# Kernel optimization log

Measured on AMD Instinct MI355X. Metric: run time of the kernel, lower is better.

The kernel has to match this reference:

```python
import jax, jax.numpy as jnp
import numpy as np

DIM = 256
GROUPS = 32
EPS = 1e-6


def setup_inputs() -> dict:
    key = jax.random.key(0)
    ks = jax.random.split(key, 7)
    B, C, H, W = 4, DIM, 64, 64
    s = 1.0 / np.sqrt(C)
    return {
        "x": jax.random.normal(ks[0], (B, C, H, W), dtype=jnp.float32),
        "gamma": jnp.ones((C,), dtype=jnp.float32),
        "beta": jnp.zeros((C,), dtype=jnp.float32),
        "w_qkv": jax.random.normal(ks[1], (3 * C, C), dtype=jnp.float32) * s,
        "b_qkv": jnp.zeros((3 * C,), dtype=jnp.float32),
        "w_proj": jax.random.normal(ks[2], (C, C), dtype=jnp.float32) * s,
        "b_proj": jnp.zeros((C,), dtype=jnp.float32),
    }


def reference(x, gamma, beta, w_qkv, b_qkv, w_proj, b_proj):
    B, C, H, W = x.shape
    N = H * W
    scale = jnp.asarray(C, x.dtype) ** 0.5

    # GroupNorm(32, C, eps=1e-6, affine)
    h = x.reshape(B, GROUPS, C // GROUPS, N)
    mu = h.mean(axis=(2, 3), keepdims=True)
    var = h.var(axis=(2, 3), keepdims=True)
    h = (h - mu) * jax.lax.rsqrt(var + EPS)
    h = h.reshape(B, C, N) * gamma[None, :, None] + beta[None, :, None]

    # 1x1 conv QKV == channel matmul
    qkv = jnp.einsum('oc,bcn->bon', w_qkv, h) + b_qkv[None, :, None]  # (B,3C,N)
    qkv = qkv.reshape(B, 3, C, N)
    q = qkv[:, 0].transpose(0, 2, 1)  # (B,N,C)
    k = qkv[:, 1].transpose(0, 2, 1)
    v = qkv[:, 2].transpose(0, 2, 1)

    attn = jnp.einsum('bqc,bkc->bqk', q, k) / scale  # (B,N,N)
    attn = jax.nn.softmax(attn, axis=-1)
    out = jnp.einsum('bqk,bkc->bqc', attn, v)  # (B,N,C)

    out = out.transpose(0, 2, 1)  # (B,C,N)
    out = jnp.einsum('oc,bcn->bon', w_proj, out) + b_proj[None, :, None]
    return x + out.reshape(B, C, H, W)
```

## Files before the change

### kernel.cpp

```cpp
#include <hip/hip_runtime.h>
#include <stdint.h>

#define DIM 256
#define NPOS 4096
#define NB 4
#define GROUPS 32

typedef __attribute__((ext_vector_type(8))) short short8;
typedef __attribute__((ext_vector_type(4))) short short4v;
typedef __attribute__((ext_vector_type(4))) float f32x4;
typedef __attribute__((ext_vector_type(16))) float f32x16;
typedef __attribute__((ext_vector_type(2))) unsigned int u32x2;
typedef __attribute__((ext_vector_type(4))) unsigned int u32x4;

__device__ __forceinline__ short f2b(float f) {
  unsigned u = __float_as_uint(f);
  unsigned r = (u + 0x7fffu + ((u >> 16) & 1u)) >> 16;
  return (short)r;
}

__device__ __forceinline__ void gl16(const short* g, char* lds) {
  __builtin_amdgcn_global_load_lds((const __attribute__((address_space(1))) void*)g,
                                   (__attribute__((address_space(3))) void*)lds, 16, 0, 0);
}

__global__ void k_convert_w(const float* __restrict__ wq, const float* __restrict__ wp,
                            short* __restrict__ wqb, short* __restrict__ wpb) {
  int i = blockIdx.x * 256 + threadIdx.x;
  if (i < 768 * 256) wqb[i] = f2b(wq[i]);
  if (i < 256 * 256) wpb[i] = f2b(wp[i]);
}

__global__ void k_gn_stats(const float* __restrict__ x, float* __restrict__ stats) {
  int bg = blockIdx.x;
  const float4* b4 = (const float4*)(x + (size_t)bg * 8 * NPOS);
  float s = 0.f, ss = 0.f;
  for (int i = threadIdx.x; i < 8192; i += 256) {
    float4 v = b4[i];
    s  += v.x + v.y + v.z + v.w;
    ss += v.x * v.x + v.y * v.y + v.z * v.z + v.w * v.w;
  }
  #pragma unroll
  for (int m = 1; m < 64; m <<= 1) { s += __shfl_xor(s, m, 64); ss += __shfl_xor(ss, m, 64); }
  __shared__ float red[8];
  int wid = threadIdx.x >> 6;
  if ((threadIdx.x & 63) == 0) { red[wid * 2] = s; red[wid * 2 + 1] = ss; }
  __syncthreads();
  if (threadIdx.x == 0) {
    float S = red[0] + red[2] + red[4] + red[6];
    float SS = red[1] + red[3] + red[5] + red[7];
    float mean = S / 32768.f;
    float var = SS / 32768.f - mean * mean;
    stats[bg * 2] = mean;
    stats[bg * 2 + 1] = rsqrtf(var + 1e-6f);
  }
}

__global__ void k_gn_apply(const float* __restrict__ x, const float* __restrict__ stats,
                           const float* __restrict__ gamma, const float* __restrict__ beta,
                           short* __restrict__ ht) {
  int ct = blockIdx.x, nt = blockIdx.y, b = blockIdx.z;
  int c0 = ct * 64, n0 = nt * 64;
  __shared__ short lt[64 * 72];
  int t = threadIdx.x;
  #pragma unroll
  for (int p = 0; p < 4; ++p) {
    int row = (t >> 4) + p * 16;
    int colb = (t & 15) * 4;
    int c = c0 + row;
    float mean = stats[(b * GROUPS + (c >> 3)) * 2];
    float rstd = stats[(b * GROUPS + (c >> 3)) * 2 + 1];
    float ga = gamma[c], be = beta[c];
    float4 v = *(const float4*)(x + ((size_t)(b * DIM + c)) * NPOS + n0 + colb);
    short4v o;
    o.x = f2b((v.x - mean) * rstd * ga + be);
    o.y = f2b((v.y - mean) * rstd * ga + be);
    o.z = f2b((v.z - mean) * rstd * ga + be);
    o.w = f2b((v.w - mean) * rstd * ga + be);
    *(short4v*)&lt[row * 72 + colb] = o;
  }
  __syncthreads();
  #pragma unroll
  for (int p = 0; p < 2; ++p) {
    int nr = (t >> 3) + p * 32;
    int ch = t & 7;
    short8 o;
    #pragma unroll
    for (int j = 0; j < 8; ++j) o[j] = lt[(ch * 8 + j) * 72 + nr];
    *(short8*)(ht + ((size_t)(b * NPOS + n0 + nr)) * DIM + c0 + ch * 8) = o;
  }
}

template <int MODE>
__launch_bounds__(256, 2)
__global__ void k_gemm(const short* __restrict__ A, const short* __restrict__ Bm,
                       const float* __restrict__ bias,
                       short* __restrict__ qb, short* __restrict__ kb, short* __restrict__ vtb,
                       const float* __restrict__ resid, float* __restrict__ outf) {
  const int K = 256;
  int b = blockIdx.z;
  int m0 = blockIdx.x * 128, n0 = blockIdx.y * 128;
  const short* Ap = (MODE == 0) ? A + (size_t)b * NPOS * K : A;
  const short* Bp = (MODE == 0) ? Bm : Bm + (size_t)b * NPOS * K;

  __shared__ short As[128 * 64], Bs[128 * 64];
  int t = threadIdx.x;
  int lane = t & 63, wid = t >> 6;
  int wm = wid >> 1, wn = wid & 1;
  f32x4 acc[4][4] = {};

  for (int kt = 0; kt < 4; ++kt) {
    int k0 = kt * 64;
    short8 av[4], bv[4];
    #pragma unroll
    for (int p = 0; p < 4; ++p) {
      int ci = t + p * 256;
      int row = ci >> 3, ch = ci & 7;
      av[p] = *(const short8*)(Ap + (size_t)(m0 + row) * K + k0 + ch * 8);
      bv[p] = *(const short8*)(Bp + (size_t)(n0 + row) * K + k0 + ch * 8);
    }
    __syncthreads();
    #pragma unroll
    for (int p = 0; p < 4; ++p) {
      int ci = t + p * 256;
      int row = ci >> 3, ch = ci & 7;
      int off = (row * 128 + ch * 16) ^ ((row & 7) << 4);
      *(short8*)((char*)As + off) = av[p];
      *(short8*)((char*)Bs + off) = bv[p];
    }
    __syncthreads();
    #pragma unroll
    for (int ks = 0; ks < 2; ++ks) {
      short8 af[4], bf[4];
      int inner = ks * 64 + (lane >> 4) * 16;
      #pragma unroll
      for (int mi = 0; mi < 4; ++mi) {
        int row = wm * 64 + mi * 16 + (lane & 15);
        af[mi] = *(short8*)((char*)As + ((row * 128 + inner) ^ ((row & 7) << 4)));
      }
      #pragma unroll
      for (int ni = 0; ni < 4; ++ni) {
        int row = wn * 64 + ni * 16 + (lane & 15);
        bf[ni] = *(short8*)((char*)Bs + ((row * 128 + inner) ^ ((row & 7) << 4)));
      }
      #pragma unroll
      for (int mi = 0; mi < 4; ++mi)
        #pragma unroll
        for (int ni = 0; ni < 4; ++ni)
          acc[mi][ni] = __builtin_amdgcn_mfma_f32_16x16x32_bf16(af[mi], bf[ni], acc[mi][ni], 0, 0, 0);
    }
  }

  #pragma unroll
  for (int mi = 0; mi < 4; ++mi)
    #pragma unroll
    for (int ni = 0; ni < 4; ++ni) {
      int gcol = n0 + wn * 64 + ni * 16 + (lane & 15);
      #pragma unroll
      for (int r = 0; r < 4; ++r) {
        int grow = m0 + wm * 64 + mi * 16 + (lane >> 4) * 4 + r;
        if (MODE == 0) {
          float v = acc[mi][ni][r] + bias[gcol];
          short h = f2b(v);
          if (gcol < 256)       qb[((size_t)b * NPOS + grow) * DIM + gcol] = h;
          else if (gcol < 512)  kb[((size_t)b * NPOS + grow) * DIM + gcol - 256] = h;
          else                  vtb[((size_t)b * DIM + gcol - 512) * NPOS + grow] = h;
        } else {
          float v = acc[mi][ni][r] + bias[grow];
          size_t idx = ((size_t)b * DIM + grow) * NPOS + gcol;
          outf[idx] = v + resid[idx];
        }
      }
    }
}

__launch_bounds__(256, 1)
__global__ void k_flash(const short* __restrict__ qb, const short* __restrict__ kb,
                        const short* __restrict__ vtb, short* __restrict__ ob) {
  __shared__ __align__(16) char smem[131072];

  int i = blockIdx.x;
  int xcd = i & 7, slot = i >> 3;
  int b = xcd >> 1;
  int bx = slot * 2 + (xcd & 1);
  int q0 = bx * 64;

  int t = threadIdx.x, lane = t & 63, wid = t >> 6;
  int q = lane & 31, hi = lane >> 5;
  int qs = wid & 1, h = wid >> 1;

  const short* kbB = kb + (size_t)b * NPOS * DIM;
  const short* vbB = vtb + (size_t)b * DIM * NPOS;

  short8 qf[16];
  {
    int qrow = q0 + qs * 32 + q;
    const short* qp = qb + ((size_t)b * NPOS + qrow) * DIM + hi * 8;
    #pragma unroll
    for (int s = 0; s < 16; ++s) {
      short8 v = *(const short8*)(qp + s * 16);
      #pragma unroll
      for (int j = 0; j < 8; ++j) {
        float f = __uint_as_float(((unsigned)(unsigned short)v[j]) << 16) * 0.0625f;
        v[j] = f2b(f);
      }
      qf[s] = v;
    }
  }

  unsigned su = h * 16384u + qs * 8192u;
  const short* srcK[8];
  const short* srcV[8];
  {
    int l5 = lane >> 5, l31 = lane & 31;
    #pragma unroll
    for (int j = 0; j < 8; ++j) {
      int r = qs * 16 + j * 2 + l5;
      int colb = (l31 * 16) ^ ((r & 7) << 4);
      srcK[j] = kbB + (size_t)(h * 2048 + r) * DIM + (colb >> 1);
      int vr = qs * 128 + j * 16 + (lane >> 2);
      int vcol = ((lane & 3) * 16) ^ ((vr & 6) << 3);
      srcV[j] = vbB + (size_t)vr * NPOS + h * 2048 + (vcol >> 1);
    }
  }

  f32x16 oacc[8] = {};
  float m = -1e30f, l = 0.f;

  const int NIT = 64;
  int buf = 0;
  #pragma unroll
  for (int j = 0; j < 8; ++j) {
    gl16(srcK[j], smem + su + j * 1024u);
    gl16(srcV[j], smem + 65536u + su + j * 1024u);
  }
  __syncthreads();

  const unsigned kx = (unsigned)((q & 7) << 4);
  const unsigned vx = (unsigned)((q & 6) << 3);

  for (int it = 0; it < NIT; ++it) {
    if (it + 1 < NIT) {
      size_t ko = (size_t)(it + 1) * 32 * DIM;
      int vo = (it + 1) * 32;
      unsigned nb = (unsigned)(buf ^ 1) * 32768u + su;
      #pragma unroll
      for (int j = 0; j < 8; ++j) {
        gl16(srcK[j] + ko, smem + nb + j * 1024u);
        gl16(srcV[j] + vo, smem + 65536u + nb + j * 1024u);
      }
    }

    const char* kl = smem + (unsigned)buf * 32768u + h * 16384u;
    const char* vl = smem + 65536u + (unsigned)buf * 32768u + h * 16384u;
    f32x16 sacc = {};
    #pragma unroll
    for (int s = 0; s < 16; ++s) {
      short8 kf = *(const short8*)(kl + q * 512u + ((s * 32u + hi * 16u) ^ kx));
      sacc = __builtin_amdgcn_mfma_f32_32x32x16_bf16(kf, qf[s], sacc, 0, 0, 0);
    }

    float mx = sacc[0];
    #pragma unroll
    for (int r = 1; r < 16; ++r) mx = fmaxf(mx, sacc[r]);
    mx = fmaxf(mx, __shfl_xor(mx, 32, 64));
    if (!__all(mx <= m + 8.f)) {
      float mn = fmaxf(m, mx);
      float al = __expf(m - mn);
      m = mn; l *= al;
      #pragma unroll
      for (int dt = 0; dt < 8; ++dt)
        #pragma unroll
        for (int r = 0; r < 16; ++r) oacc[dt][r] *= al;
    }
    float p_[16];
    float ts = 0.f;
    #pragma unroll
    for (int r = 0; r < 16; ++r) { p_[r] = __expf(sacc[r] - m); ts += p_[r]; }
    ts += __shfl_xor(ts, 32, 64);
    l += ts;

    unsigned w0, w1, w2, w3, w4, w5, w6, w7;
    asm("v_cvt_pk_bf16_f32 %0, %1, %2" : "=v"(w0) : "v"(p_[0]),  "v"(p_[1]));
    asm("v_cvt_pk_bf16_f32 %0, %1, %2" : "=v"(w1) : "v"(p_[2]),  "v"(p_[3]));
    asm("v_cvt_pk_bf16_f32 %0, %1, %2" : "=v"(w2) : "v"(p_[4]),  "v"(p_[5]));
    asm("v_cvt_pk_bf16_f32 %0, %1, %2" : "=v"(w3) : "v"(p_[6]),  "v"(p_[7]));
    asm("v_cvt_pk_bf16_f32 %0, %1, %2" : "=v"(w4) : "v"(p_[8]),  "v"(p_[9]));
    asm("v_cvt_pk_bf16_f32 %0, %1, %2" : "=v"(w5) : "v"(p_[10]), "v"(p_[11]));
    asm("v_cvt_pk_bf16_f32 %0, %1, %2" : "=v"(w6) : "v"(p_[12]), "v"(p_[13]));
    asm("v_cvt_pk_bf16_f32 %0, %1, %2" : "=v"(w7) : "v"(p_[14]), "v"(p_[15]));
    asm("v_permlane32_swap_b32 %0, %1" : "+v"(w0), "+v"(w2));
    asm("v_permlane32_swap_b32 %0, %1" : "+v"(w1), "+v"(w3));
    asm("v_permlane32_swap_b32 %0, %1" : "+v"(w4), "+v"(w6));
    asm("v_permlane32_swap_b32 %0, %1" : "+v"(w5), "+v"(w7));
    short8 pf0 = __builtin_bit_cast(short8, (u32x4){w0, w1, w2, w3});
    short8 pf1 = __builtin_bit_cast(short8, (u32x4){w4, w5, w6, w7});

    #pragma unroll
    for (int dt = 0; dt < 8; ++dt) {
      unsigned vrow = (dt * 32u + q) * 64u;
      short8 vf0 = *(const short8*)(vl + vrow + ((hi * 16u) ^ vx));
      short8 vf1 = *(const short8*)(vl + vrow + ((32u + hi * 16u) ^ vx));
      oacc[dt] = __builtin_amdgcn_mfma_f32_32x32x16_bf16(vf0, pf0, oacc[dt], 0, 0, 0);
      oacc[dt] = __builtin_amdgcn_mfma_f32_32x32x16_bf16(vf1, pf1, oacc[dt], 0, 0, 0);
    }
    __syncthreads();
    buf ^= 1;
  }

  float* lmm = (float*)(smem + 100352);
  float* lml = lmm + 128;
  if (lane < 32) { lmm[(qs * 2 + h) * 32 + q] = m; lml[(qs * 2 + h) * 32 + q] = l; }
  __syncthreads();
  float mo = lmm[(qs * 2 + (h ^ 1)) * 32 + q];
  float lo = lml[(qs * 2 + (h ^ 1)) * 32 + q];
  float M = fmaxf(m, mo);
  float al = __expf(m - M);
  float Lf = l * al + lo * __expf(mo - M);
  float iL = 1.f / Lf;

  float* sc32 = (float*)smem;
  short* sc16 = (short*)(smem + 66560);
  if (h == 0) {
    #pragma unroll
    for (int dt = 0; dt < 8; ++dt)
      #pragma unroll
      for (int r = 0; r < 16; ++r) {
        int d = dt * 32 + (r & 3) + 8 * (r >> 2) + 4 * hi;
        sc32[qs * 8224 + q * 257 + d] = oacc[dt][r] * al;
      }
  }
  __syncthreads();
  if (h == 1) {
    #pragma unroll
    for (int dt = 0; dt < 8; ++dt)
      #pragma unroll
      for (int r = 0; r < 16; ++r) {
        int d = dt * 32 + (r & 3) + 8 * (r >> 2) + 4 * hi;
        float v = (sc32[qs * 8224 + q * 257 + d] + oacc[dt][r] * al) * iL;
        sc16[qs * 8256 + q * 258 + d] = f2b(v);
      }
  }
  __syncthreads();
  {
    int row = t >> 2;
    const short* src = sc16 + (row >> 5) * 8256 + (row & 31) * 258 + (t & 3) * 64;
    short* dst = ob + ((size_t)b * NPOS + q0 + row) * DIM + (t & 3) * 64;
    #pragma unroll
    for (int j = 0; j < 8; ++j)
      *(short8*)(dst + j * 8) = *(const short8*)(src + j * 8);
  }
}

extern "C" void kernel_launch(void* const* d_in, const int* in_sizes, int n_in,
                              void* d_out, int out_size, void* d_ws, size_t ws_size,
                              hipStream_t stream) {
  const float* x     = (const float*)d_in[0];
  const float* gamma = (const float*)d_in[1];
  const float* beta  = (const float*)d_in[2];
  const float* wqkv  = (const float*)d_in[3];
  const float* bqkv  = (const float*)d_in[4];
  const float* wproj = (const float*)d_in[5];
  const float* bproj = (const float*)d_in[6];
  float* out = (float*)d_out;

  char* ws = (char*)d_ws;
  float* stats = (float*)ws;
  short* wqb = (short*)(ws + 1024);
  short* wpb = (short*)(ws + 1024 + 393216);
  size_t off = 1024 + 393216 + 131072;
  const size_t SZ = (size_t)NB * NPOS * DIM * sizeof(short);
  short* ht   = (short*)(ws + off); off += SZ;
  short* qbuf = (short*)(ws + off); off += SZ;
  short* kbuf = (short*)(ws + off); off += SZ;
  short* vtb  = (short*)(ws + off); off += SZ;
  short* obuf = ht;

  k_convert_w<<<768, 256, 0, stream>>>(wqkv, wproj, wqb, wpb);
  k_gn_stats<<<128, 256, 0, stream>>>(x, stats);
  k_gn_apply<<<dim3(4, 64, NB), 256, 0, stream>>>(x, stats, gamma, beta, ht);
  k_gemm<0><<<dim3(32, 6, NB), 256, 0, stream>>>(ht, wqb, bqkv, qbuf, kbuf, vtb, nullptr, nullptr);
  k_flash<<<dim3(256), 256, 0, stream>>>(qbuf, kbuf, vtb, obuf);
  k_gemm<1><<<dim3(2, 32, NB), 256, 0, stream>>>(wpb, obuf, bproj, nullptr, nullptr, nullptr, x, out);
}
```

Baseline: 176.1 us.

## Split flash attention head dimension across two wave groups with 512-thread blocks

Doubles the flash-attention block to 8 waves, splitting the V/output head dimension into two halves so each wave holds 4 output accumulator tiles instead of 8. K/V tile loads are redistributed across all 512 threads, and the final merge and store are adapted to the new layout. This lowers per-wave register pressure and raises waves per CU for better latency hiding. In exchange, each QK^T score tile and its softmax are computed twice, once by each half. The launch_bounds minimum-blocks hint of 2 cannot be met given the 128KB shared-memory allocation.

```diff
diff --git a/kernel.cpp b/kernel.cpp
--- a/kernel.cpp
+++ b/kernel.cpp
@@ -174,7 +174,7 @@
     }
 }
 
-__launch_bounds__(256, 1)
+__launch_bounds__(512, 2)
 __global__ void k_flash(const short* __restrict__ qb, const short* __restrict__ kb,
                         const short* __restrict__ vtb, short* __restrict__ ob) {
   __shared__ __align__(16) char smem[131072];
@@ -187,7 +187,7 @@
 
   int t = threadIdx.x, lane = t & 63, wid = t >> 6;
   int q = lane & 31, hi = lane >> 5;
-  int qs = wid & 1, h = wid >> 1;
+  int qs = wid & 1, h = (wid >> 1) & 1, ds = wid >> 2;
 
   const short* kbB = kb + (size_t)b * NPOS * DIM;
   const short* vbB = vtb + (size_t)b * DIM * NPOS;
@@ -208,31 +208,32 @@
     }
   }
 
-  unsigned su = h * 16384u + qs * 8192u;
-  const short* srcK[8];
-  const short* srcV[8];
-  {
-    int l5 = lane >> 5, l31 = lane & 31;
-    #pragma unroll
-    for (int j = 0; j < 8; ++j) {
-      int r = qs * 16 + j * 2 + l5;
-      int colb = (l31 * 16) ^ ((r & 7) << 4);
-      srcK[j] = kbB + (size_t)(h * 2048 + r) * DIM + (colb >> 1);
-      int vr = qs * 128 + j * 16 + (lane >> 2);
-      int vcol = ((lane & 3) * 16) ^ ((vr & 6) << 3);
-      srcV[j] = vbB + (size_t)vr * NPOS + h * 2048 + (vcol >> 1);
-    }
-  }
-
-  f32x16 oacc[8] = {};
+  const short* srcK[4];
+  const short* srcV[4];
+  unsigned dstK[4], dstV[4];
+  #pragma unroll
+  for (int j = 0; j < 4; ++j) {
+    int c = wid * 4 + j;
+    int ch = c >> 4;
+    int kr = (c & 15) * 2 + (lane >> 5);
+    int kcol = ((lane & 31) * 16) ^ ((kr & 7) << 4);
+    srcK[j] = kbB + (size_t)(ch * 2048 + kr) * DIM + (kcol >> 1);
+    int dr = (c & 15) * 16 + (lane >> 2);
+    int vcol = ((lane & 3) * 16) ^ ((dr & 6) << 3);
+    srcV[j] = vbB + (size_t)dr * NPOS + ch * 2048 + (vcol >> 1);
+    dstK[j] = (unsigned)c * 1024u;
+    dstV[j] = 65536u + (unsigned)c * 1024u;
+  }
+
+  f32x16 oacc[4] = {};
   float m = -1e30f, l = 0.f;
 
   const int NIT = 64;
   int buf = 0;
   #pragma unroll
-  for (int j = 0; j < 8; ++j) {
-    gl16(srcK[j], smem + su + j * 1024u);
-    gl16(srcV[j], smem + 65536u + su + j * 1024u);
+  for (int j = 0; j < 4; ++j) {
+    gl16(srcK[j], smem + dstK[j]);
+    gl16(srcV[j], smem + dstV[j]);
   }
   __syncthreads();
 
@@ -243,11 +244,11 @@
     if (it + 1 < NIT) {
       size_t ko = (size_t)(it + 1) * 32 * DIM;
       int vo = (it + 1) * 32;
-      unsigned nb = (unsigned)(buf ^ 1) * 32768u + su;
-      #pragma unroll
-      for (int j = 0; j < 8; ++j) {
-        gl16(srcK[j] + ko, smem + nb + j * 1024u);
-        gl16(srcV[j] + vo, smem + 65536u + nb + j * 1024u);
+      unsigned nb = (unsigned)(buf ^ 1) * 32768u;
+      #pragma unroll
+      for (int j = 0; j < 4; ++j) {
+        gl16(srcK[j] + ko, smem + nb + dstK[j]);
+        gl16(srcV[j] + vo, smem + nb + dstV[j]);
       }
     }
 
@@ -269,7 +270,7 @@
       float al = __expf(m - mn);
       m = mn; l *= al;
       #pragma unroll
-      for (int dt = 0; dt < 8; ++dt)
+      for (int dt = 0; dt < 4; ++dt)
         #pragma unroll
         for (int r = 0; r < 16; ++r) oacc[dt][r] *= al;
     }
@@ -297,12 +298,12 @@
     short8 pf1 = __builtin_bit_cast(short8, (u32x4){w4, w5, w6, w7});
 
     #pragma unroll
-    for (int dt = 0; dt < 8; ++dt) {
-      unsigned vrow = (dt * 32u + q) * 64u;
+    for (int dtl = 0; dtl < 4; ++dtl) {
+      unsigned vrow = ((ds * 4 + dtl) * 32u + q) * 64u;
       short8 vf0 = *(const short8*)(vl + vrow + ((hi * 16u) ^ vx));
       short8 vf1 = *(const short8*)(vl + vrow + ((32u + hi * 16u) ^ vx));
-      oacc[dt] = __builtin_amdgcn_mfma_f32_32x32x16_bf16(vf0, pf0, oacc[dt], 0, 0, 0);
-      oacc[dt] = __builtin_amdgcn_mfma_f32_32x32x16_bf16(vf1, pf1, oacc[dt], 0, 0, 0);
+      oacc[dtl] = __builtin_amdgcn_mfma_f32_32x32x16_bf16(vf0, pf0, oacc[dtl], 0, 0, 0);
+      oacc[dtl] = __builtin_amdgcn_mfma_f32_32x32x16_bf16(vf1, pf1, oacc[dtl], 0, 0, 0);
     }
     __syncthreads();
     buf ^= 1;
@@ -310,7 +311,7 @@
 
   float* lmm = (float*)(smem + 100352);
   float* lml = lmm + 128;
-  if (lane < 32) { lmm[(qs * 2 + h) * 32 + q] = m; lml[(qs * 2 + h) * 32 + q] = l; }
+  if (ds == 0 && lane < 32) { lmm[(qs * 2 + h) * 32 + q] = m; lml[(qs * 2 + h) * 32 + q] = l; }
   __syncthreads();
   float mo = lmm[(qs * 2 + (h ^ 1)) * 32 + q];
   float lo = lml[(qs * 2 + (h ^ 1)) * 32 + q];
@@ -323,31 +324,31 @@
   short* sc16 = (short*)(smem + 66560);
   if (h == 0) {
     #pragma unroll
-    for (int dt = 0; dt < 8; ++dt)
+    for (int dtl = 0; dtl < 4; ++dtl)
       #pragma unroll
       for (int r = 0; r < 16; ++r) {
-        int d = dt * 32 + (r & 3) + 8 * (r >> 2) + 4 * hi;
-        sc32[qs * 8224 + q * 257 + d] = oacc[dt][r] * al;
+        int d = (ds * 4 + dtl) * 32 + (r & 3) + 8 * (r >> 2) + 4 * hi;
+        sc32[qs * 8224 + q * 257 + d] = oacc[dtl][r] * al;
       }
   }
   __syncthreads();
   if (h == 1) {
     #pragma unroll
-    for (int dt = 0; dt < 8; ++dt)
+    for (int dtl = 0; dtl < 4; ++dtl)
       #pragma unroll
       for (int r = 0; r < 16; ++r) {
-        int d = dt * 32 + (r & 3) + 8 * (r >> 2) + 4 * hi;
-        float v = (sc32[qs * 8224 + q * 257 + d] + oacc[dt][r] * al) * iL;
+        int d = (ds * 4 + dtl) * 32 + (r & 3) + 8 * (r >> 2) + 4 * hi;
+        float v = (sc32[qs * 8224 + q * 257 + d] + oacc[dtl][r] * al) * iL;
         sc16[qs * 8256 + q * 258 + d] = f2b(v);
       }
   }
   __syncthreads();
   {
-    int row = t >> 2;
-    const short* src = sc16 + (row >> 5) * 8256 + (row & 31) * 258 + (t & 3) * 64;
-    short* dst = ob + ((size_t)b * NPOS + q0 + row) * DIM + (t & 3) * 64;
-    #pragma unroll
-    for (int j = 0; j < 8; ++j)
+    int row = t >> 3;
+    const short* src = sc16 + (row >> 5) * 8256 + (row & 31) * 258 + (t & 7) * 32;
+    short* dst = ob + ((size_t)b * NPOS + q0 + row) * DIM + (t & 7) * 32;
+    #pragma unroll
+    for (int j = 0; j < 4; ++j)
       *(short8*)(dst + j * 8) = *(const short8*)(src + j * 8);
   }
 }
@@ -380,6 +381,6 @@
   k_gn_stats<<<128, 256, 0, stream>>>(x, stats);
   k_gn_apply<<<dim3(4, 64, NB), 256, 0, stream>>>(x, stats, gamma, beta, ht);
   k_gemm<0><<<dim3(32, 6, NB), 256, 0, stream>>>(ht, wqb, bqkv, qbuf, kbuf, vtb, nullptr, nullptr);
-  k_flash<<<dim3(256), 256, 0, stream>>>(qbuf, kbuf, vtb, obuf);
+  k_flash<<<dim3(256), 512, 0, stream>>>(qbuf, kbuf, vtb, obuf);
   k_gemm<1><<<dim3(2, 32, NB), 256, 0, stream>>>(wpb, obuf, bproj, nullptr, nullptr, nullptr, x, out);
 }
```

After: 182.5 us. 3.6% more time.

## Load V fragments directly into registers instead of staging through LDS

Applied to the files above, without the earlier changes.

The V tile is no longer staged in shared memory via global_load_lds. Each lane now loads its own V MFMA operands straight from global memory into a double-buffered register array (vA/vB), and the loop is unrolled by two to alternate the buffers. The aim is to remove the LDS traffic for V reads and shrink shared memory use. In exchange, register pressure grows by 32 short8 values, and the per-lane global V loads are less coalesced (16-byte chunks strided by NPOS rows).

```diff
diff --git a/kernel.cpp b/kernel.cpp
--- a/kernel.cpp
+++ b/kernel.cpp
@@ -177,7 +177,7 @@
 __launch_bounds__(256, 1)
 __global__ void k_flash(const short* __restrict__ qb, const short* __restrict__ kb,
                         const short* __restrict__ vtb, short* __restrict__ ob) {
-  __shared__ __align__(16) char smem[131072];
+  __shared__ __align__(16) char smem[101376];
 
   int i = blockIdx.x;
   int xcd = i & 7, slot = i >> 3;
@@ -210,7 +210,6 @@
 
   unsigned su = h * 16384u + qs * 8192u;
   const short* srcK[8];
-  const short* srcV[8];
   {
     int l5 = lane >> 5, l31 = lane & 31;
     #pragma unroll
@@ -218,95 +217,97 @@
       int r = qs * 16 + j * 2 + l5;
       int colb = (l31 * 16) ^ ((r & 7) << 4);
       srcK[j] = kbB + (size_t)(h * 2048 + r) * DIM + (colb >> 1);
-      int vr = qs * 128 + j * 16 + (lane >> 2);
-      int vcol = ((lane & 3) * 16) ^ ((vr & 6) << 3);
-      srcV[j] = vbB + (size_t)vr * NPOS + h * 2048 + (vcol >> 1);
-    }
-  }
+    }
+  }
+
+  const short* vbase = vbB + (size_t)q * NPOS + h * 2048 + hi * 8;
 
   f32x16 oacc[8] = {};
   float m = -1e30f, l = 0.f;
+  short8 vA[16], vB[16];
 
   const int NIT = 64;
   int buf = 0;
   #pragma unroll
-  for (int j = 0; j < 8; ++j) {
-    gl16(srcK[j], smem + su + j * 1024u);
-    gl16(srcV[j], smem + 65536u + su + j * 1024u);
+  for (int j = 0; j < 8; ++j) gl16(srcK[j], smem + su + j * 1024u);
+  #pragma unroll
+  for (int dt = 0; dt < 8; ++dt) {
+    vA[2 * dt]     = *(const short8*)(vbase + (size_t)dt * 32 * NPOS);
+    vA[2 * dt + 1] = *(const short8*)(vbase + (size_t)dt * 32 * NPOS + 16);
   }
   __syncthreads();
 
   const unsigned kx = (unsigned)((q & 7) << 4);
-  const unsigned vx = (unsigned)((q & 6) << 3);
-
-  for (int it = 0; it < NIT; ++it) {
-    if (it + 1 < NIT) {
-      size_t ko = (size_t)(it + 1) * 32 * DIM;
-      int vo = (it + 1) * 32;
-      unsigned nb = (unsigned)(buf ^ 1) * 32768u + su;
-      #pragma unroll
-      for (int j = 0; j < 8; ++j) {
-        gl16(srcK[j] + ko, smem + nb + j * 1024u);
-        gl16(srcV[j] + vo, smem + 65536u + nb + j * 1024u);
-      }
-    }
-
-    const char* kl = smem + (unsigned)buf * 32768u + h * 16384u;
-    const char* vl = smem + 65536u + (unsigned)buf * 32768u + h * 16384u;
-    f32x16 sacc = {};
-    #pragma unroll
-    for (int s = 0; s < 16; ++s) {
-      short8 kf = *(const short8*)(kl + q * 512u + ((s * 32u + hi * 16u) ^ kx));
-      sacc = __builtin_amdgcn_mfma_f32_32x32x16_bf16(kf, qf[s], sacc, 0, 0, 0);
-    }
-
-    float mx = sacc[0];
-    #pragma unroll
-    for (int r = 1; r < 16; ++r) mx = fmaxf(mx, sacc[r]);
-    mx = fmaxf(mx, __shfl_xor(mx, 32, 64));
-    if (!__all(mx <= m + 8.f)) {
-      float mn = fmaxf(m, mx);
-      float al = __expf(m - mn);
-      m = mn; l *= al;
-      #pragma unroll
-      for (int dt = 0; dt < 8; ++dt)
-        #pragma unroll
-        for (int r = 0; r < 16; ++r) oacc[dt][r] *= al;
-    }
-    float p_[16];
-    float ts = 0.f;
-    #pragma unroll
-    for (int r = 0; r < 16; ++r) { p_[r] = __expf(sacc[r] - m); ts += p_[r]; }
-    ts += __shfl_xor(ts, 32, 64);
-    l += ts;
-
-    unsigned w0, w1, w2, w3, w4, w5, w6, w7;
-    asm("v_cvt_pk_bf16_f32 %0, %1, %2" : "=v"(w0) : "v"(p_[0]),  "v"(p_[1]));
-    asm("v_cvt_pk_bf16_f32 %0, %1, %2" : "=v"(w1) : "v"(p_[2]),  "v"(p_[3]));
-    asm("v_cvt_pk_bf16_f32 %0, %1, %2" : "=v"(w2) : "v"(p_[4]),  "v"(p_[5]));
-    asm("v_cvt_pk_bf16_f32 %0, %1, %2" : "=v"(w3) : "v"(p_[6]),  "v"(p_[7]));
-    asm("v_cvt_pk_bf16_f32 %0, %1, %2" : "=v"(w4) : "v"(p_[8]),  "v"(p_[9]));
-    asm("v_cvt_pk_bf16_f32 %0, %1, %2" : "=v"(w5) : "v"(p_[10]), "v"(p_[11]));
-    asm("v_cvt_pk_bf16_f32 %0, %1, %2" : "=v"(w6) : "v"(p_[12]), "v"(p_[13]));
-    asm("v_cvt_pk_bf16_f32 %0, %1, %2" : "=v"(w7) : "v"(p_[14]), "v"(p_[15]));
-    asm("v_permlane32_swap_b32 %0, %1" : "+v"(w0), "+v"(w2));
-    asm("v_permlane32_swap_b32 %0, %1" : "+v"(w1), "+v"(w3));
-    asm("v_permlane32_swap_b32 %0, %1" : "+v"(w4), "+v"(w6));
-    asm("v_permlane32_swap_b32 %0, %1" : "+v"(w5), "+v"(w7));
-    short8 pf0 = __builtin_bit_cast(short8, (u32x4){w0, w1, w2, w3});
-    short8 pf1 = __builtin_bit_cast(short8, (u32x4){w4, w5, w6, w7});
-
-    #pragma unroll
-    for (int dt = 0; dt < 8; ++dt) {
-      unsigned vrow = (dt * 32u + q) * 64u;
-      short8 vf0 = *(const short8*)(vl + vrow + ((hi * 16u) ^ vx));
-      short8 vf1 = *(const short8*)(vl + vrow + ((32u + hi * 16u) ^ vx));
-      oacc[dt] = __builtin_amdgcn_mfma_f32_32x32x16_bf16(vf0, pf0, oacc[dt], 0, 0, 0);
-      oacc[dt] = __builtin_amdgcn_mfma_f32_32x32x16_bf16(vf1, pf1, oacc[dt], 0, 0, 0);
-    }
-    __syncthreads();
-    buf ^= 1;
-  }
+
+#define FITER(IT, VC, VN)                                                          \
+  {                                                                                \
+    if ((IT) + 1 < NIT) {                                                          \
+      size_t ko = (size_t)((IT) + 1) * 32 * DIM;                                   \
+      unsigned nb = (unsigned)(buf ^ 1) * 32768u + su;                             \
+      _Pragma("unroll")                                                            \
+      for (int j = 0; j < 8; ++j) gl16(srcK[j] + ko, smem + nb + j * 1024u);       \
+      const short* vb2 = vbase + ((IT) + 1) * 32;                                  \
+      _Pragma("unroll")                                                            \
+      for (int dt = 0; dt < 8; ++dt) {                                             \
+        VN[2 * dt]     = *(const short8*)(vb2 + (size_t)dt * 32 * NPOS);           \
+        VN[2 * dt + 1] = *(const short8*)(vb2 + (size_t)dt * 32 * NPOS + 16);      \
+      }                                                                            \
+    }                                                                              \
+    const char* kl = smem + (unsigned)buf * 32768u + h * 16384u;                   \
+    f32x16 sacc = {};                                                              \
+    _Pragma("unroll")                                                              \
+    for (int s = 0; s < 16; ++s) {                                                 \
+      short8 kf = *(const short8*)(kl + q * 512u + ((s * 32u + hi * 16u) ^ kx));   \
+      sacc = __builtin_amdgcn_mfma_f32_32x32x16_bf16(kf, qf[s], sacc, 0, 0, 0);    \
+    }                                                                              \
+    float mx = sacc[0];                                                            \
+    _Pragma("unroll")                                                              \
+    for (int r = 1; r < 16; ++r) mx = fmaxf(mx, sacc[r]);                          \
+    mx = fmaxf(mx, __shfl_xor(mx, 32, 64));                                        \
+    if (!__all(mx <= m + 8.f)) {                                                   \
+      float mn = fmaxf(m, mx);                                                     \
+      float al = __expf(m - mn);                                                   \
+      m = mn; l *= al;                                                             \
+      _Pragma("unroll")                                                            \
+      for (int dt = 0; dt < 8; ++dt)                                               \
+        _Pragma("unroll")                                                          \
+        for (int r = 0; r < 16; ++r) oacc[dt][r] *= al;                            \
+    }                                                                              \
+    float p_[16];                                                                  \
+    float ts = 0.f;                                                                \
+    _Pragma("unroll")                                                              \
+    for (int r = 0; r < 16; ++r) { p_[r] = __expf(sacc[r] - m); ts += p_[r]; }     \
+    ts += __shfl_xor(ts, 32, 64);                                                  \
+    l += ts;                                                                       \
+    unsigned w0, w1, w2, w3, w4, w5, w6, w7;                                       \
+    asm("v_cvt_pk_bf16_f32 %0, %1, %2" : "=v"(w0) : "v"(p_[0]),  "v"(p_[1]));      \
+    asm("v_cvt_pk_bf16_f32 %0, %1, %2" : "=v"(w1) : "v"(p_[2]),  "v"(p_[3]));      \
+    asm("v_cvt_pk_bf16_f32 %0, %1, %2" : "=v"(w2) : "v"(p_[4]),  "v"(p_[5]));      \
+    asm("v_cvt_pk_bf16_f32 %0, %1, %2" : "=v"(w3) : "v"(p_[6]),  "v"(p_[7]));      \
+    asm("v_cvt_pk_bf16_f32 %0, %1, %2" : "=v"(w4) : "v"(p_[8]),  "v"(p_[9]));      \
+    asm("v_cvt_pk_bf16_f32 %0, %1, %2" : "=v"(w5) : "v"(p_[10]), "v"(p_[11]));     \
+    asm("v_cvt_pk_bf16_f32 %0, %1, %2" : "=v"(w6) : "v"(p_[12]), "v"(p_[13]));     \
+    asm("v_cvt_pk_bf16_f32 %0, %1, %2" : "=v"(w7) : "v"(p_[14]), "v"(p_[15]));     \
+    asm("v_permlane32_swap_b32 %0, %1" : "+v"(w0), "+v"(w2));                      \
+    asm("v_permlane32_swap_b32 %0, %1" : "+v"(w1), "+v"(w3));                      \
+    asm("v_permlane32_swap_b32 %0, %1" : "+v"(w4), "+v"(w6));                      \
+    asm("v_permlane32_swap_b32 %0, %1" : "+v"(w5), "+v"(w7));                      \
+    short8 pf0 = __builtin_bit_cast(short8, (u32x4){w0, w1, w2, w3});              \
+    short8 pf1 = __builtin_bit_cast(short8, (u32x4){w4, w5, w6, w7});              \
+    _Pragma("unroll")                                                              \
+    for (int dt = 0; dt < 8; ++dt) {                                               \
+      oacc[dt] = __builtin_amdgcn_mfma_f32_32x32x16_bf16(VC[2*dt],   pf0, oacc[dt], 0, 0, 0); \
+      oacc[dt] = __builtin_amdgcn_mfma_f32_32x32x16_bf16(VC[2*dt+1], pf1, oacc[dt], 0, 0, 0); \
+    }                                                                              \
+    __syncthreads();                                                               \
+    buf ^= 1;                                                                      \
+  }
+
+  for (int it = 0; it < NIT; it += 2) {
+    FITER(it, vA, vB)
+    FITER(it + 1, vB, vA)
+  }
+#undef FITER
 
   float* lmm = (float*)(smem + 100352);
   float* lml = lmm + 128;
```

After: 266.7 us. 51.4% more time.
